# Optimization experiments

Measured on AMD Instinct MI355X. Metric: run time of the kernel, lower is better.

Reference implementation:

```python
import jax, jax.numpy as jnp
import numpy as np
from jax import lax
import math

B, C, H, W = 2, 128, 128, 256
K = 3
KK = K * K
AUX = C + 5

def conv2d(x, w, b, pad):
    out = lax.conv_general_dilated(x, w, (1, 1), [(pad, pad), (pad, pad)],
                                   dimension_numbers=('NCHW', 'OIHW', 'NCHW'))
    return out + b[None, :, None, None]

def erp_coord(h, w):
    xs = jnp.linspace(-math.pi, math.pi, w)
    ys = jnp.linspace(-math.pi / 2, math.pi / 2, h)
    theta = jnp.broadcast_to(xs[None, :], (h, w))
    phi = jnp.broadcast_to(ys[:, None], (h, w))
    return jnp.stack([jnp.sin(theta), jnp.cos(theta), jnp.sin(phi), jnp.cos(phi)], 0)[None]

def freq_energy(x, h, w):
    mag = jnp.abs(jnp.fft.rfft2(x, norm='ortho')).mean(1, keepdims=True)
    # bilinear resize (align_corners=False, half-pixel) to (h, w)
    return jax.image.resize(mag, (x.shape[0], 1, h, w), method='linear', antialias=False)

def deform_sample(x, offset):
    # x: (b,c,H,W); offset: (b, 2*KK, H, W)
    b, c, h, w = x.shape
    off = offset.reshape(b, KK, 2, h, w)
    xx = jnp.arange(w, dtype=x.dtype)[None, None, None, :]
    yy = jnp.arange(h, dtype=x.dtype)[None, None, :, None]
    # align_corners=True normalize/unnormalize cancels exactly
    px = xx + off[:, :, 0]  # (b,KK,h,w)
    py = yy + off[:, :, 1]
    x0 = jnp.floor(px).astype(jnp.int32); x1 = x0 + 1
    y0 = jnp.floor(py).astype(jnp.int32); y1 = y0 + 1
    wx1 = px - x0.astype(x.dtype); wx0 = 1.0 - wx1
    wy1 = py - y0.astype(x.dtype); wy0 = 1.0 - wy1
    flat = x.reshape(b, c, h * w)

    def gather(ix, iy):
        valid = ((ix >= 0) & (ix < w) & (iy >= 0) & (iy < h)).astype(x.dtype)
        idx = jnp.clip(iy, 0, h - 1) * w + jnp.clip(ix, 0, w - 1)  # (b,KK,h,w)
        g = jax.vmap(lambda f, i: f[:, i])(flat, idx)  # (b,c,KK,h,w)
        return g * valid[:, None]

    out = (gather(x0, y0) * (wx0 * wy0)[:, None]
           + gather(x1, y0) * (wx1 * wy0)[:, None]
           + gather(x0, y1) * (wx0 * wy1)[:, None]
           + gather(x1, y1) * (wx1 * wy1)[:, None])
    return out.reshape(b, c * KK, h, w)

def setup_inputs() -> dict:
    key = jax.random.key(0)
    ks = jax.random.split(key, 12)
    s = lambda *sh: 1.0 / np.sqrt(np.prod(sh[1:]))
    def unif(k, *sh):
        return jax.random.uniform(k, sh, jnp.float32, -s(*sh), s(*sh))
    return {
        'x': jax.random.normal(ks[0], (B, C, H, W), jnp.float32),
        'offset_w': unif(ks[1], 2 * KK, AUX, 3, 3),
        'offset_b': jnp.zeros((2 * KK,), jnp.float32),
        'gate_w1': unif(ks[2], AUX // 2, AUX, 3, 3),
        'gate_b1': jnp.zeros((AUX // 2,), jnp.float32),
        'gate_w2': unif(ks[3], 1, AUX // 2, 1, 1),
        'gate_b2': jnp.zeros((1,), jnp.float32),
        'base_w': unif(ks[4], C, C, K, K),
        'base_b': jnp.zeros((C,), jnp.float32),
        'def_w': jax.random.normal(ks[5], (C, C, K, K), jnp.float32) * s(C, C, K, K),
        'def_b': jnp.zeros((C,), jnp.float32),
    }

def reference(x, offset_w, offset_b, gate_w1, gate_b1, gate_w2, gate_b2,
              base_w, base_b, def_w, def_b):
    b, c, h, w = x.shape
    coord = jnp.broadcast_to(erp_coord(h, w), (b, 4, h, w)).astype(x.dtype)
    fe = freq_energy(x, h, w)
    aux = jnp.concatenate([x, coord, fe], 1)
    offset = conv2d(aux, offset_w, offset_b, 1)
    g = jax.nn.relu(conv2d(aux, gate_w1, gate_b1, 1))
    gate = jax.nn.sigmoid(conv2d(g, gate_w2, gate_b2, 0))
    y_base = conv2d(x, base_w, base_b, K // 2)
    sampled = deform_sample(x, offset)  # (b, c*KK, h, w)
    y_def = conv2d(sampled, def_w.reshape(c, c * KK, 1, 1), def_b, 0)
    return (1.0 - gate) * y_base + gate * y_def
```

## Files before the change

kernel.cpp:

```cpp
#include <hip/hip_runtime.h>
#include <hip/hip_bf16.h>

#define BB 2
#define CC 128
#define HH 128
#define WW 256
#define HWs (HH*WW)
#define PI_F 3.14159265358979323846f

typedef __attribute__((ext_vector_type(8))) short bf16x8;
typedef __attribute__((ext_vector_type(8))) unsigned short u16x8;
typedef __attribute__((ext_vector_type(4))) float f32x4;

__device__ __forceinline__ ushort f2bf(float f) {
  uint u = __float_as_uint(f);
  u = (u + 0x7fffu + ((u >> 16) & 1u)) >> 16;
  return (ushort)u;
}
__device__ __forceinline__ uint f2bf_fast(float f) {
  return (__float_as_uint(f) + 0x8000u) >> 16;
}
__device__ __forceinline__ float bf2f(ushort u) {
  return __uint_as_float(((uint)u) << 16);
}

__global__ __launch_bounds__(256) void pack_all_kernel(
    const float* __restrict__ bw, const float* __restrict__ dw,
    const float* __restrict__ ow, const float* __restrict__ gw,
    ushort* __restrict__ apkF, ushort* __restrict__ apkA,
    ushort* __restrict__ a1, ushort* __restrict__ a2) {
  int bid = blockIdx.x;
  int tid = threadIdx.x;
  if (bid < 144) {
    int gid = bid * 256 + tid;
    int lane = gid & 63;
    int kf = (gid >> 6) & 3;
    int mf = (gid >> 8) & 7;
    int chunk = gid >> 11;
    int part = chunk >= 9;
    int tap = part ? chunk - 9 : chunk;
    int m = mf * 16 + (lane & 15);
    int cb = kf * 32 + ((lane >> 4) << 3);
    const float* src = part ? dw : bw;
    ushort* dst = apkF + (size_t)gid * 8;
#pragma unroll
    for (int j = 0; j < 8; ++j)
      dst[j] = f2bf(src[(size_t)m * 1152 + (size_t)(cb + j) * 9 + tap]);
  } else if (bid < 212) {
    int gid = (bid - 144) * 256 + tid;
    if (gid >= 17280) return;
    int lane = gid & 63;
    int kf = (gid >> 6) % 5;
    int mf = (gid / 320) % 6;
    int tap = gid / 1920;
    int m = mf * 16 + (lane & 15);
    int cb = kf * 32 + ((lane >> 4) << 3);
#pragma unroll
    for (int j = 0; j < 8; ++j) {
      int c = cb + j;
      float v = 0.f;
      if (c < 133) {
        if (m < 18) v = ow[(size_t)m * 1197 + c * 9 + tap];
        else if (m < 84) v = gw[(size_t)(m - 18) * 1197 + c * 9 + tap];
      }
      apkA[(size_t)gid * 8 + j] = f2bf(v);
    }
  } else {
    int gid = (bid - 212) * 256 + tid;
    if (gid < 10240) {
      int lane = gid & 63, kf = (gid >> 6) & 7, mf = gid >> 9;
      int m = mf * 16 + (lane & 15);
      int kk0 = kf * 32 + ((lane >> 4) << 3);
#pragma unroll
      for (int j = 0; j < 8; ++j) {
        int kk = kk0 + j;
        float v = 0.f;
        if (m < 129)      { int tt = (m * kk) & 255;         v =  cosf(tt * (PI_F / 128.f)); }
        else if (m < 258) { int tt = ((m - 129) * kk) & 255; v = -sinf(tt * (PI_F / 128.f)); }
        a1[(size_t)gid * 8 + j] = f2bf(v);
      }
    } else if (gid < 18432) {
      int q = gid - 10240;
      int lane = q & 63, kf = (q >> 6) & 7, mf = q >> 9;
      int m = mf * 16 + (lane & 15);
      int g = m & 127;
      int kk0 = kf * 32 + ((lane >> 4) << 3);
#pragma unroll
      for (int j = 0; j < 8; ++j) {
        int kk = kk0 + j;
        int h2 = kk & 127;
        int tt = (g * h2) & 127;
        float ang = tt * (PI_F / 64.f);
        float v = (m < 128) ? ((kk < 128) ? cosf(ang) : sinf(ang))
                            : ((kk < 128) ? -sinf(ang) : cosf(ang));
        a2[(size_t)q * 8 + j] = f2bf(v);
      }
    }
  }
}

__global__ __launch_bounds__(256) void xt_kernel(const float* __restrict__ x,
    ushort* __restrict__ xt) {
  __shared__ ushort sT[64][128];
  int blk = blockIdx.x;
  int b = blk >> 7, h = blk & 127;
  int t = threadIdx.x;
  const float* xb = x + ((size_t)b * CC * HH + h) * WW;
  ushort* ob = xt + (((size_t)b * HH + h) * WW) * 128;
  for (int wt = 0; wt < 4; ++wt) {
    __syncthreads();
    {
      int w = t & 63;
      int sw = (w & 7) << 3;
#pragma unroll
      for (int it = 0; it < 4; ++it) {
        int oct = (t >> 6) + it * 4;
        u16x8 v;
#pragma unroll
        for (int j = 0; j < 8; ++j)
          v[j] = f2bf(xb[(size_t)(oct * 8 + j) * HWs + wt * 64 + w]);
        *(u16x8*)&sT[w][(oct << 3) ^ sw] = v;
      }
    }
    __syncthreads();
#pragma unroll
    for (int it = 0; it < 4; ++it) {
      int u = t + it * 256;
      int w = u >> 4, oct = u & 15;
      u16x8 v = *(const u16x8*)&sT[w][(oct << 3) ^ ((w & 7) << 3)];
      *(u16x8*)&ob[(size_t)(wt * 64 + w) * 128 + oct * 8] = v;
    }
  }
}

__global__ __launch_bounds__(256) void dft1_kernel(const float* __restrict__ x,
    const ushort* __restrict__ a1pk, ushort* __restrict__ F1) {
  int bc = blockIdx.x;
  int t = threadIdx.x, lane = t & 63, wv = t >> 6;
  int q8 = (lane >> 4) << 3, rq = (lane >> 4) << 2;
  const bf16x8* APK = (const bf16x8*)a1pk;
  ushort* f1b = F1 + (size_t)bc * 36864;
  for (int nh = 0; nh < 2; ++nh) {
    f32x4 acc[5][4];
#pragma unroll
    for (int i = 0; i < 5; ++i)
#pragma unroll
      for (int n = 0; n < 4; ++n) acc[i][n] = (f32x4){0.f, 0.f, 0.f, 0.f};
    for (int kf = 0; kf < 8; ++kf) {
      bf16x8 av[5];
#pragma unroll
      for (int i = 0; i < 5; ++i)
        av[i] = APK[(size_t)((wv * 5 + i) * 8 + kf) * 64 + lane];
#pragma unroll
      for (int n2 = 0; n2 < 4; ++n2) {
        int nf = nh * 4 + n2;
        int hh = nf * 16 + (lane & 15);
        const float* xp = x + (((size_t)bc * HH + hh) << 8) + kf * 32 + q8;
        float4 xa = *(const float4*)xp;
        float4 xb4 = *(const float4*)(xp + 4);
        bf16x8 bv;
        bv[0] = (short)f2bf(xa.x); bv[1] = (short)f2bf(xa.y);
        bv[2] = (short)f2bf(xa.z); bv[3] = (short)f2bf(xa.w);
        bv[4] = (short)f2bf(xb4.x); bv[5] = (short)f2bf(xb4.y);
        bv[6] = (short)f2bf(xb4.z); bv[7] = (short)f2bf(xb4.w);
#pragma unroll
        for (int i = 0; i < 5; ++i)
          acc[i][n2] = __builtin_amdgcn_mfma_f32_16x16x32_bf16(av[i], bv, acc[i][n2], 0, 0, 0);
      }
    }
#pragma unroll
    for (int n2 = 0; n2 < 4; ++n2) {
      int hh = (nh * 4 + n2) * 16 + (lane & 15);
#pragma unroll
      for (int i = 0; i < 5; ++i) {
#pragma unroll
        for (int r = 0; r < 4; ++r) {
          int m = (wv * 5 + i) * 16 + rq + r;
          if (m < 258) {
            int sel = m >= 129;
            int k = sel ? m - 129 : m;
            f1b[(size_t)k * 256 + sel * 128 + hh] = f2bf(acc[i][n2][r]);
          }
        }
      }
    }
  }
}

__global__ __launch_bounds__(256) void dft2_kernel(const ushort* __restrict__ F1,
    const ushort* __restrict__ a2pk, float* __restrict__ magbuf) {
  int bc = blockIdx.x;
  int t = threadIdx.x, lane = t & 63, wv = t >> 6;
  int q8 = (lane >> 4) << 3, rq = (lane >> 4) << 2;
  const bf16x8* APK = (const bf16x8*)a2pk;
  const ushort* f1b = F1 + (size_t)bc * 36864;
  float* mb = magbuf + (size_t)bc * 18432;
  for (int ng = 0; ng < 3; ++ng) {
    f32x4 acc[4][3];
#pragma unroll
    for (int i = 0; i < 4; ++i)
#pragma unroll
      for (int n = 0; n < 3; ++n) acc[i][n] = (f32x4){0.f, 0.f, 0.f, 0.f};
    for (int kf = 0; kf < 8; ++kf) {
      bf16x8 av[4];
#pragma unroll
      for (int i = 0; i < 4; ++i) {
        int mf = (i < 2) ? (2 * wv + i) : (2 * wv + (i - 2) + 8);
        av[i] = APK[(size_t)(mf * 8 + kf) * 64 + lane];
      }
#pragma unroll
      for (int n2 = 0; n2 < 3; ++n2) {
        int nf = ng * 3 + n2;
        int krow = nf * 16 + (lane & 15);
        bf16x8 bv = *(const bf16x8*)&f1b[(size_t)krow * 256 + kf * 32 + q8];
#pragma unroll
        for (int i = 0; i < 4; ++i)
          acc[i][n2] = __builtin_amdgcn_mfma_f32_16x16x32_bf16(av[i], bv, acc[i][n2], 0, 0, 0);
      }
    }
#pragma unroll
    for (int n2 = 0; n2 < 3; ++n2) {
      int k = (ng * 3 + n2) * 16 + (lane & 15);
      if (k < 129) {
#pragma unroll
        for (int pr = 0; pr < 2; ++pr) {
#pragma unroll
          for (int r = 0; r < 4; ++r) {
            int g = (2 * wv + pr) * 16 + rq + r;
            float vr = acc[pr][n2][r], vi = acc[pr + 2][n2][r];
            mb[(size_t)g * 144 + k] = sqrtf(vr * vr + vi * vi);
          }
        }
      }
    }
  }
}

__global__ __launch_bounds__(256) void fe_reduce_kernel(const float* __restrict__ magbuf,
    float* __restrict__ fe) {
  int i = blockIdx.x * 256 + threadIdx.x;
  if (i >= 36864) return;
  int k = i % 144;
  int gb = i / 144;
  int g = gb & 127, b = gb >> 7;
  if (k >= 129) return;
  const float* mp = magbuf + (size_t)b * 128 * 18432 + (size_t)g * 144 + k;
  float s = 0.f;
  for (int c = 0; c < 128; ++c) s += mp[(size_t)c * 18432];
  fe[((size_t)b * 128 + g) * 129 + k] = s * (1.0f / (181.01933598375618f * 128.0f));
}

__global__ __launch_bounds__(256) void aux_conv_kernel(
    const ushort* __restrict__ xt, const float* __restrict__ fe,
    const ushort* __restrict__ apk,
    const float* __restrict__ offset_b, const float* __restrict__ gate_b1,
    const float* __restrict__ w2, const float* __restrict__ b2,
    float* __restrict__ offs, float* __restrict__ gate) {
  __shared__ ushort Bt[64][168];
  __shared__ float gld[66][64];
  __shared__ float2 thS[66];
  __shared__ float2 phS[3];
  __shared__ float feS[3][66];
  int t = threadIdx.x;
  int bid = blockIdx.x;
  int lin = (bid & 7) * 128 + (bid >> 3);
  int bz = lin >> 9;
  int rest = lin & 511;
  int h = rest >> 2, w0 = (rest & 3) << 6;
  int lane = t & 63, wid = t >> 6;
  int wm = wid >> 1, wn = wid & 1;
  int q8 = (lane >> 4) << 3, rq = (lane >> 4) << 2;

  if (t < 66) {
    float th = -PI_F + (float)(w0 + t - 1) * (2.0f * PI_F / 255.0f);
    thS[t] = make_float2(sinf(th), cosf(th));
  }
  if (t < 3) {
    float ph = -0.5f * PI_F + (float)(h + t - 1) * (PI_F / 127.0f);
    phS[t] = make_float2(sinf(ph), cosf(ph));
  }
  if (t < 198) {
    int gyi = t / 66, gxi = t % 66;
    int gy = h + gyi - 1, gx = w0 + gxi - 1;
    float v = 0.f;
    if (gy >= 0 && gy < HH && gx >= 0 && gx < WW) {
      float sxc = ((float)gx + 0.5f) * (129.0f / 256.0f) - 0.5f;
      float fx = floorf(sxc);
      int x0 = (int)fx;
      float fr = sxc - fx;
      int x1 = min(x0 + 1, 128);
      x0 = max(x0, 0);
      const float* fb = fe + ((size_t)bz * 128 + gy) * 129;
      v = fb[x0] * (1.f - fr) + fb[x1] * fr;
    }
    feS[gyi][gxi] = v;
  }

  f32x4 acc[3][2];
#pragma unroll
  for (int i = 0; i < 3; ++i) {
    acc[i][0] = (f32x4){0.f, 0.f, 0.f, 0.f};
    acc[i][1] = (f32x4){0.f, 0.f, 0.f, 0.f};
  }
  int p0 = wn * 32 + (lane & 15), p1 = p0 + 16;
  const bf16x8* APK = (const bf16x8*)apk;
  const ushort* xtb = xt + (size_t)bz * 4194304;

  for (int tap = 0; tap < 9; ++tap) {
    int ky = tap / 3 - 1, kx = tap % 3 - 1;
    int gy = h + ky;
    __syncthreads();
    for (int u = t; u < 1280; u += 256) {
      int oct = u >> 6, p = u & 63;
      int gx = w0 + p + kx;
      bool okp = (gy >= 0) && (gy < HH) && ((unsigned)gx < 256u);
      u16x8 v = (u16x8){0, 0, 0, 0, 0, 0, 0, 0};
      if (oct < 16) {
        if (okp) v = *(const u16x8*)&xtb[((((size_t)gy << 8) + gx) << 7) + (oct << 3)];
      } else if (oct == 16) {
        if (okp) {
          float2 tc = thS[p + kx + 1];
          float2 pc = phS[ky + 1];
          float fv = feS[ky + 1][p + kx + 1];
          v[0] = f2bf(tc.x); v[1] = f2bf(tc.y);
          v[2] = f2bf(pc.x); v[3] = f2bf(pc.y);
          v[4] = f2bf(fv);
        }
      }
      *(u16x8*)&Bt[p][oct << 3] = v;
    }
    __syncthreads();
    int fb = (tap * 6 + wm * 3) * 5;
#pragma unroll
    for (int kf = 0; kf < 5; ++kf) {
      int ko = kf * 32 + q8;
      bf16x8 b0 = *(const bf16x8*)&Bt[p0][ko];
      bf16x8 b1 = *(const bf16x8*)&Bt[p1][ko];
#pragma unroll
      for (int mfi = 0; mfi < 3; ++mfi) {
        bf16x8 av = APK[(size_t)(fb + mfi * 5 + kf) * 64 + lane];
        acc[mfi][0] = __builtin_amdgcn_mfma_f32_16x16x32_bf16(av, b0, acc[mfi][0], 0, 0, 0);
        acc[mfi][1] = __builtin_amdgcn_mfma_f32_16x16x32_bf16(av, b1, acc[mfi][1], 0, 0, 0);
      }
    }
  }
#pragma unroll
  for (int nf = 0; nf < 2; ++nf) {
    int p = wn * 32 + nf * 16 + (lane & 15);
    int w = w0 + p;
#pragma unroll
    for (int mfi = 0; mfi < 3; ++mfi) {
#pragma unroll
      for (int r = 0; r < 4; ++r) {
        int oc = wm * 48 + mfi * 16 + rq + r;
        float v = acc[mfi][nf][r];
        if (oc < 18) {
          offs[((size_t)bz * 18 + oc) * HWs + h * WW + w] = v + offset_b[oc];
        } else if (oc < 84) {
          gld[oc - 18][p] = fmaxf(v + gate_b1[oc - 18], 0.f);
        }
      }
    }
  }
  __syncthreads();
  if (t < 64) {
    float s = b2[0];
    for (int c = 0; c < 66; ++c) s = fmaf(gld[c][t], w2[c], s);
    gate[(size_t)bz * HWs + h * WW + w0 + t] = 1.f / (1.f + expf(-s));
  }
}

__global__ __launch_bounds__(256) void fused_out_kernel(
    const ushort* __restrict__ xt, const float* __restrict__ offsp,
    const ushort* __restrict__ apk,
    const float* __restrict__ base_b, const float* __restrict__ def_b,
    const float* __restrict__ gate, float* __restrict__ out) {
  __shared__ ushort Win[4 * 68 * 64];
  __shared__ ushort Bt[2][64][64];
  __shared__ float gvS[64];
  __shared__ float bbS[128], bdS[128];
  int t = threadIdx.x;
  int bid = blockIdx.x;
  int lin = (bid & 7) * 128 + (bid >> 3);
  int bz = lin >> 9;
  int rest = lin & 511;
  int h = rest >> 2, w0 = (rest & 3) << 6;
  int lane = t & 63, wv = t >> 6;
  int l15 = lane & 15, lg = lane >> 4;
  int rq = lg << 2;
  const ushort* xtb = xt + (size_t)bz * 4194304;
  const bf16x8* APK = (const bf16x8*)apk;
  const u16x8 zv = (u16x8){0, 0, 0, 0, 0, 0, 0, 0};

  if (t < 64) gvS[t] = gate[(size_t)bz * HWs + h * WW + w0 + t];
  else if (t < 192) {
    int c = t - 64;
    bbS[c] = base_b[c];
    bdS[c] = def_b[c];
  }

  int p = t & 63, o4 = t >> 6;
  int mw = w0 + p;
  float oxr[9], oyr[9];
#pragma unroll
  for (int d = 0; d < 9; ++d) {
    oxr[d] = offsp[((size_t)bz * 18 + 2 * d) * HWs + h * WW + mw];
    oyr[d] = offsp[((size_t)bz * 18 + 2 * d + 1) * HWs + h * WW + mw];
  }

  f32x4 accB[2][4], accD[2][4];
#pragma unroll
  for (int mi = 0; mi < 2; ++mi)
#pragma unroll
    for (int nf = 0; nf < 4; ++nf) {
      accB[mi][nf] = (f32x4){0.f, 0.f, 0.f, 0.f};
      accD[mi][nf] = (f32x4){0.f, 0.f, 0.f, 0.f};
    }

  for (int half = 0; half < 2; ++half) {
#pragma unroll
    for (int it = 0; it < 9; ++it) {
      int u = it * 256 + t;
      if (u < 2176) {
        int s = u & 7;
        int c = (u >> 3) % 68;
        int r = u / 544;
        int gy = h - 1 + r, gx = w0 - 2 + c;
        u16x8 v = zv;
        if ((unsigned)gy < 128u && (unsigned)gx < 256u)
          v = *(const u16x8*)&xtb[((((size_t)gy << 8) + gx) << 7) + (half << 6) + (s << 3)];
        *(u16x8*)&Win[((r * 68 + c) << 6) + ((s ^ (c & 7)) << 3)] = v;
      }
    }
    __syncthreads();

    auto stage = [&](int nb, int d) {
      float px = (float)mw + oxr[d], py = (float)h + oyr[d];
      float fx = floorf(px), fy = floorf(py);
      int x0 = (int)fx, y0 = (int)fy;
      float wx1 = px - fx, wy1 = py - fy;
      float wx0 = 1.f - wx1, wy0 = 1.f - wy1;
      int x1 = x0 + 1, y1 = y0 + 1;
      bool vx0 = (unsigned)x0 < 256u, vx1 = (unsigned)x1 < 256u;
      bool vy0 = (unsigned)y0 < 128u, vy1 = (unsigned)y1 < 128u;
      float g0 = (vx0 && vy0) ? wx0 * wy0 : 0.f;
      float g1 = (vx1 && vy0) ? wx1 * wy0 : 0.f;
      float g2 = (vx0 && vy1) ? wx0 * wy1 : 0.f;
      float g3 = (vx1 && vy1) ? wx1 * wy1 : 0.f;
      int cx0 = min(max(x0, 0), 255), cx1 = min(max(x1, 0), 255);
      int cy0 = min(max(y0, 0), 127), cy1 = min(max(y1, 0), 127);
      int rx0 = cx0 - w0 + 2, rx1 = cx1 - w0 + 2;
      int ry0 = cy0 - h + 1,  ry1 = cy1 - h + 1;
      bool i00 = ((unsigned)ry0 < 4u) && ((unsigned)rx0 < 68u);
      bool i01 = ((unsigned)ry0 < 4u) && ((unsigned)rx1 < 68u);
      bool i10 = ((unsigned)ry1 < 4u) && ((unsigned)rx0 < 68u);
      bool i11 = ((unsigned)ry1 < 4u) && ((unsigned)rx1 < 68u);
#pragma unroll
      for (int oo = 0; oo < 2; ++oo) {
        int o = o4 + oo * 4;
        u16x8 v00, v01, v10, v11;
        if (i00) v00 = *(const u16x8*)&Win[((ry0 * 68 + rx0) << 6) + ((o ^ (rx0 & 7)) << 3)];
        else     v00 = *(const u16x8*)&xtb[((((size_t)cy0 << 8) + cx0) << 7) + (half << 6) + (o << 3)];
        if (i01) v01 = *(const u16x8*)&Win[((ry0 * 68 + rx1) << 6) + ((o ^ (rx1 & 7)) << 3)];
        else     v01 = *(const u16x8*)&xtb[((((size_t)cy0 << 8) + cx1) << 7) + (half << 6) + (o << 3)];
        if (i10) v10 = *(const u16x8*)&Win[((ry1 * 68 + rx0) << 6) + ((o ^ (rx0 & 7)) << 3)];
        else     v10 = *(const u16x8*)&xtb[((((size_t)cy1 << 8) + cx0) << 7) + (half << 6) + (o << 3)];
        if (i11) v11 = *(const u16x8*)&Win[((ry1 * 68 + rx1) << 6) + ((o ^ (rx1 & 7)) << 3)];
        else     v11 = *(const u16x8*)&xtb[((((size_t)cy1 << 8) + cx1) << 7) + (half << 6) + (o << 3)];
        uint pk[4];
#pragma unroll
        for (int i = 0; i < 4; ++i) {
          float f0 = bf2f(v00[2 * i]) * g0 + bf2f(v01[2 * i]) * g1
                   + bf2f(v10[2 * i]) * g2 + bf2f(v11[2 * i]) * g3;
          float f1 = bf2f(v00[2 * i + 1]) * g0 + bf2f(v01[2 * i + 1]) * g1
                   + bf2f(v10[2 * i + 1]) * g2 + bf2f(v11[2 * i + 1]) * g3;
          pk[i] = f2bf_fast(f0) | (f2bf_fast(f1) << 16);
        }
        *(uint4*)&Bt[nb][p][(o ^ (p & 7)) << 3] = make_uint4(pk[0], pk[1], pk[2], pk[3]);
      }
    };

    stage(0, 0);
    __syncthreads();

    int buf = 0;
    for (int d = 0; d < 9; ++d) {
      int ky = d / 3 - 1, kx = d % 3 - 1;
      int ryB = ky + 1;
#pragma unroll
      for (int kfi = 0; kfi < 2; ++kfi) {
        int kff = half * 2 + kfi;
        int segk = kfi * 4 + lg;
        bf16x8 aB0 = APK[(size_t)((d * 8 + wv) * 4 + kff) * 64 + lane];
        bf16x8 aB1 = APK[(size_t)((d * 8 + wv + 4) * 4 + kff) * 64 + lane];
        bf16x8 aD0 = APK[(size_t)(((9 + d) * 8 + wv) * 4 + kff) * 64 + lane];
        bf16x8 aD1 = APK[(size_t)(((9 + d) * 8 + wv + 4) * 4 + kff) * 64 + lane];
#pragma unroll
        for (int nf = 0; nf < 4; ++nf) {
          int pix = nf * 16 + l15;
          int cxr = pix + kx + 2;
          bf16x8 bB = *(const bf16x8*)&Win[((ryB * 68 + cxr) << 6) + ((segk ^ (cxr & 7)) << 3)];
          bf16x8 bD = *(const bf16x8*)&Bt[buf][pix][(segk ^ (pix & 7)) << 3];
          accB[0][nf] = __builtin_amdgcn_mfma_f32_16x16x32_bf16(aB0, bB, accB[0][nf], 0, 0, 0);
          accB[1][nf] = __builtin_amdgcn_mfma_f32_16x16x32_bf16(aB1, bB, accB[1][nf], 0, 0, 0);
          accD[0][nf] = __builtin_amdgcn_mfma_f32_16x16x32_bf16(aD0, bD, accD[0][nf], 0, 0, 0);
          accD[1][nf] = __builtin_amdgcn_mfma_f32_16x16x32_bf16(aD1, bD, accD[1][nf], 0, 0, 0);
        }
      }
      if (d < 8) stage(buf ^ 1, d + 1);
      __syncthreads();
      buf ^= 1;
    }
    if (half == 0) __syncthreads();
  }

#pragma unroll
  for (int nf = 0; nf < 4; ++nf) {
    int pix = nf * 16 + l15;
    float gv = gvS[pix], go = 1.f - gv;
    int w = w0 + pix;
#pragma unroll
    for (int mi = 0; mi < 2; ++mi) {
      int mf = wv + mi * 4;
#pragma unroll
      for (int r = 0; r < 4; ++r) {
        int oc = mf * 16 + rq + r;
        out[(((size_t)bz * CC + oc) << 15) + h * WW + w] =
            go * (accB[mi][nf][r] + bbS[oc]) + gv * (accD[mi][nf][r] + bdS[oc]);
      }
    }
  }
}

extern "C" void kernel_launch(void* const* d_in, const int* in_sizes, int n_in,
                              void* d_out, int out_size, void* d_ws, size_t ws_size,
                              hipStream_t stream) {
  const float* x        = (const float*)d_in[0];
  const float* offset_w = (const float*)d_in[1];
  const float* offset_b = (const float*)d_in[2];
  const float* gate_w1  = (const float*)d_in[3];
  const float* gate_b1  = (const float*)d_in[4];
  const float* gate_w2  = (const float*)d_in[5];
  const float* gate_b2  = (const float*)d_in[6];
  const float* base_w   = (const float*)d_in[7];
  const float* base_b   = (const float*)d_in[8];
  const float* def_w    = (const float*)d_in[9];
  const float* def_b    = (const float*)d_in[10];
  float* out = (float*)d_out;
  float* ws  = (float*)d_ws;

  float* offsb   = ws;
  float* gatebuf = offsb + 1179648;
  float* fe      = gatebuf + 65536;
  float* magbuf  = fe + 33024;
  ushort* xt     = (ushort*)(magbuf + 4718592);
  ushort* F1     = xt + 16777216;
  ushort* a1pk   = F1 + 9437184;
  ushort* a2pk   = a1pk + 81920;
  ushort* apkF   = a2pk + 65536;
  ushort* apkA   = apkF + 294912;

  pack_all_kernel<<<284, 256, 0, stream>>>(base_w, def_w, offset_w, gate_w1,
                                           apkF, apkA, a1pk, a2pk);
  xt_kernel<<<256, 256, 0, stream>>>(x, xt);

  dft1_kernel<<<256, 256, 0, stream>>>(x, a1pk, F1);
  dft2_kernel<<<256, 256, 0, stream>>>(F1, a2pk, magbuf);
  fe_reduce_kernel<<<144, 256, 0, stream>>>(magbuf, fe);

  aux_conv_kernel<<<1024, 256, 0, stream>>>(xt, fe, apkA, offset_b, gate_b1,
                                            gate_w2, gate_b2, offsb, gatebuf);

  fused_out_kernel<<<1024, 256, 0, stream>>>(xt, offsb, apkF, base_b, def_b,
                                             gatebuf, out);
}
```

Measured before the change: 196.8 us.

## Compute deformable samples directly into MFMA B-fragments, dropping shared staging buffer

The fused output kernel no longer stages bilinear-sampled values into a double-buffered shared tile with per-tap barriers. Each wave now computes the sampled B operands for its own pixels in registers and feeds them straight to MFMA. The warp tiling changes to 2x2 (64 channels by 32 pixels per wave), and offsets are cached in shared memory. This removes 9 barriers per half and the shared write/read round-trip, but each wave pair now repeats the sampling for its pixel columns, so gather and interpolation work is done twice.

```diff
diff --git a/kernel.cpp b/kernel.cpp
--- a/kernel.cpp
+++ b/kernel.cpp
@@ -376,7 +376,7 @@
     const float* __restrict__ base_b, const float* __restrict__ def_b,
     const float* __restrict__ gate, float* __restrict__ out) {
   __shared__ ushort Win[4 * 68 * 64];
-  __shared__ ushort Bt[2][64][64];
+  __shared__ float offS[9][2][64];
   __shared__ float gvS[64];
   __shared__ float bbS[128], bdS[128];
   int t = threadIdx.x;
@@ -386,6 +386,7 @@
   int rest = lin & 511;
   int h = rest >> 2, w0 = (rest & 3) << 6;
   int lane = t & 63, wv = t >> 6;
+  int wm = wv >> 1, wn = wv & 1;
   int l15 = lane & 15, lg = lane >> 4;
   int rq = lg << 2;
   const ushort* xtb = xt + (size_t)bz * 4194304;
@@ -398,26 +399,24 @@
     bbS[c] = base_b[c];
     bdS[c] = def_b[c];
   }
-
-  int p = t & 63, o4 = t >> 6;
-  int mw = w0 + p;
-  float oxr[9], oyr[9];
-#pragma unroll
-  for (int d = 0; d < 9; ++d) {
-    oxr[d] = offsp[((size_t)bz * 18 + 2 * d) * HWs + h * WW + mw];
-    oyr[d] = offsp[((size_t)bz * 18 + 2 * d + 1) * HWs + h * WW + mw];
-  }
-
-  f32x4 accB[2][4], accD[2][4];
-#pragma unroll
-  for (int mi = 0; mi < 2; ++mi)
-#pragma unroll
-    for (int nf = 0; nf < 4; ++nf) {
-      accB[mi][nf] = (f32x4){0.f, 0.f, 0.f, 0.f};
-      accD[mi][nf] = (f32x4){0.f, 0.f, 0.f, 0.f};
+  for (int u = t; u < 1152; u += 256) {
+    int d = u >> 7, r = (u >> 6) & 1, p = u & 63;
+    offS[d][r][p] = offsp[((size_t)bz * 18 + 2 * d + r) * HWs + h * WW + w0 + p];
+  }
+
+  int pix0 = wn * 32 + l15;
+
+  f32x4 acc[4][2][2];
+#pragma unroll
+  for (int i = 0; i < 4; ++i)
+#pragma unroll
+    for (int n = 0; n < 2; ++n) {
+      acc[i][n][0] = (f32x4){0.f, 0.f, 0.f, 0.f};
+      acc[i][n][1] = (f32x4){0.f, 0.f, 0.f, 0.f};
     }
 
   for (int half = 0; half < 2; ++half) {
+    if (half) __syncthreads();
 #pragma unroll
     for (int it = 0; it < 9; ++it) {
       int u = it * 256 + t;
@@ -434,99 +433,108 @@
     }
     __syncthreads();
 
-    auto stage = [&](int nb, int d) {
-      float px = (float)mw + oxr[d], py = (float)h + oyr[d];
-      float fx = floorf(px), fy = floorf(py);
-      int x0 = (int)fx, y0 = (int)fy;
-      float wx1 = px - fx, wy1 = py - fy;
-      float wx0 = 1.f - wx1, wy0 = 1.f - wy1;
-      int x1 = x0 + 1, y1 = y0 + 1;
-      bool vx0 = (unsigned)x0 < 256u, vx1 = (unsigned)x1 < 256u;
-      bool vy0 = (unsigned)y0 < 128u, vy1 = (unsigned)y1 < 128u;
-      float g0 = (vx0 && vy0) ? wx0 * wy0 : 0.f;
-      float g1 = (vx1 && vy0) ? wx1 * wy0 : 0.f;
-      float g2 = (vx0 && vy1) ? wx0 * wy1 : 0.f;
-      float g3 = (vx1 && vy1) ? wx1 * wy1 : 0.f;
-      int cx0 = min(max(x0, 0), 255), cx1 = min(max(x1, 0), 255);
-      int cy0 = min(max(y0, 0), 127), cy1 = min(max(y1, 0), 127);
-      int rx0 = cx0 - w0 + 2, rx1 = cx1 - w0 + 2;
-      int ry0 = cy0 - h + 1,  ry1 = cy1 - h + 1;
-      bool i00 = ((unsigned)ry0 < 4u) && ((unsigned)rx0 < 68u);
-      bool i01 = ((unsigned)ry0 < 4u) && ((unsigned)rx1 < 68u);
-      bool i10 = ((unsigned)ry1 < 4u) && ((unsigned)rx0 < 68u);
-      bool i11 = ((unsigned)ry1 < 4u) && ((unsigned)rx1 < 68u);
-#pragma unroll
-      for (int oo = 0; oo < 2; ++oo) {
-        int o = o4 + oo * 4;
-        u16x8 v00, v01, v10, v11;
-        if (i00) v00 = *(const u16x8*)&Win[((ry0 * 68 + rx0) << 6) + ((o ^ (rx0 & 7)) << 3)];
-        else     v00 = *(const u16x8*)&xtb[((((size_t)cy0 << 8) + cx0) << 7) + (half << 6) + (o << 3)];
-        if (i01) v01 = *(const u16x8*)&Win[((ry0 * 68 + rx1) << 6) + ((o ^ (rx1 & 7)) << 3)];
-        else     v01 = *(const u16x8*)&xtb[((((size_t)cy0 << 8) + cx1) << 7) + (half << 6) + (o << 3)];
-        if (i10) v10 = *(const u16x8*)&Win[((ry1 * 68 + rx0) << 6) + ((o ^ (rx0 & 7)) << 3)];
-        else     v10 = *(const u16x8*)&xtb[((((size_t)cy1 << 8) + cx0) << 7) + (half << 6) + (o << 3)];
-        if (i11) v11 = *(const u16x8*)&Win[((ry1 * 68 + rx1) << 6) + ((o ^ (rx1 & 7)) << 3)];
-        else     v11 = *(const u16x8*)&xtb[((((size_t)cy1 << 8) + cx1) << 7) + (half << 6) + (o << 3)];
-        uint pk[4];
-#pragma unroll
-        for (int i = 0; i < 4; ++i) {
-          float f0 = bf2f(v00[2 * i]) * g0 + bf2f(v01[2 * i]) * g1
-                   + bf2f(v10[2 * i]) * g2 + bf2f(v11[2 * i]) * g3;
-          float f1 = bf2f(v00[2 * i + 1]) * g0 + bf2f(v01[2 * i + 1]) * g1
-                   + bf2f(v10[2 * i + 1]) * g2 + bf2f(v11[2 * i + 1]) * g3;
-          pk[i] = f2bf_fast(f0) | (f2bf_fast(f1) << 16);
-        }
-        *(uint4*)&Bt[nb][p][(o ^ (p & 7)) << 3] = make_uint4(pk[0], pk[1], pk[2], pk[3]);
-      }
-    };
-
-    stage(0, 0);
-    __syncthreads();
-
-    int buf = 0;
     for (int d = 0; d < 9; ++d) {
       int ky = d / 3 - 1, kx = d % 3 - 1;
-      int ryB = ky + 1;
+      float g[2][4];
+      int wb[2][4];
+      int gb[2][4];
+      bool inw[2][4];
+#pragma unroll
+      for (int nf = 0; nf < 2; ++nf) {
+        int pix = pix0 + nf * 16;
+        float ox = offS[d][0][pix], oy = offS[d][1][pix];
+        float px = (float)(w0 + pix) + ox, py = (float)h + oy;
+        float fx = floorf(px), fy = floorf(py);
+        int x0 = (int)fx, y0 = (int)fy;
+        float wx1 = px - fx, wy1 = py - fy;
+        float wx0 = 1.f - wx1, wy0 = 1.f - wy1;
+        int x1 = x0 + 1, y1 = y0 + 1;
+        bool vx0 = (unsigned)x0 < 256u, vx1 = (unsigned)x1 < 256u;
+        bool vy0 = (unsigned)y0 < 128u, vy1 = (unsigned)y1 < 128u;
+        g[nf][0] = (vx0 && vy0) ? wx0 * wy0 : 0.f;
+        g[nf][1] = (vx1 && vy0) ? wx1 * wy0 : 0.f;
+        g[nf][2] = (vx0 && vy1) ? wx0 * wy1 : 0.f;
+        g[nf][3] = (vx1 && vy1) ? wx1 * wy1 : 0.f;
+        int cx0 = min(max(x0, 0), 255), cx1 = min(max(x1, 0), 255);
+        int cy0 = min(max(y0, 0), 127), cy1 = min(max(y1, 0), 127);
+        int rx0 = cx0 - w0 + 2, rx1 = cx1 - w0 + 2;
+        int ry0 = cy0 - h + 1,  ry1 = cy1 - h + 1;
+        inw[nf][0] = ((unsigned)ry0 < 4u) && ((unsigned)rx0 < 68u);
+        inw[nf][1] = ((unsigned)ry0 < 4u) && ((unsigned)rx1 < 68u);
+        inw[nf][2] = ((unsigned)ry1 < 4u) && ((unsigned)rx0 < 68u);
+        inw[nf][3] = ((unsigned)ry1 < 4u) && ((unsigned)rx1 < 68u);
+        wb[nf][0] = ((ry0 * 68 + rx0) << 6) ^ ((rx0 & 7) << 3);
+        wb[nf][1] = ((ry0 * 68 + rx1) << 6) ^ ((rx1 & 7) << 3);
+        wb[nf][2] = ((ry1 * 68 + rx0) << 6) ^ ((rx0 & 7) << 3);
+        wb[nf][3] = ((ry1 * 68 + rx1) << 6) ^ ((rx1 & 7) << 3);
+        gb[nf][0] = (((cy0 << 8) + cx0) << 7) + (half << 6);
+        gb[nf][1] = (((cy0 << 8) + cx1) << 7) + (half << 6);
+        gb[nf][2] = (((cy1 << 8) + cx0) << 7) + (half << 6);
+        gb[nf][3] = (((cy1 << 8) + cx1) << 7) + (half << 6);
+      }
 #pragma unroll
       for (int kfi = 0; kfi < 2; ++kfi) {
+        int o = kfi * 4 + lg;
+        int o8 = o << 3;
+        bf16x8 bD[2], bB[2];
+#pragma unroll
+        for (int nf = 0; nf < 2; ++nf) {
+          u16x8 cv[4];
+#pragma unroll
+          for (int c = 0; c < 4; ++c) {
+            if (inw[nf][c]) cv[c] = *(const u16x8*)&Win[wb[nf][c] ^ o8];
+            else            cv[c] = *(const u16x8*)&xtb[gb[nf][c] + o8];
+          }
+          uint pk[4];
+#pragma unroll
+          for (int i = 0; i < 4; ++i) {
+            float f0 = bf2f(cv[0][2 * i]) * g[nf][0] + bf2f(cv[1][2 * i]) * g[nf][1]
+                     + bf2f(cv[2][2 * i]) * g[nf][2] + bf2f(cv[3][2 * i]) * g[nf][3];
+            float f1 = bf2f(cv[0][2 * i + 1]) * g[nf][0] + bf2f(cv[1][2 * i + 1]) * g[nf][1]
+                     + bf2f(cv[2][2 * i + 1]) * g[nf][2] + bf2f(cv[3][2 * i + 1]) * g[nf][3];
+            pk[i] = f2bf_fast(f0) | (f2bf_fast(f1) << 16);
+          }
+          uint4 tmp = make_uint4(pk[0], pk[1], pk[2], pk[3]);
+          bD[nf] = *(const bf16x8*)&tmp;
+          int cxr = pix0 + nf * 16 + kx + 2;
+          bB[nf] = *(const bf16x8*)&Win[(((ky + 1) * 68 + cxr) << 6) + ((o ^ (cxr & 7)) << 3)];
+        }
         int kff = half * 2 + kfi;
-        int segk = kfi * 4 + lg;
-        bf16x8 aB0 = APK[(size_t)((d * 8 + wv) * 4 + kff) * 64 + lane];
-        bf16x8 aB1 = APK[(size_t)((d * 8 + wv + 4) * 4 + kff) * 64 + lane];
-        bf16x8 aD0 = APK[(size_t)(((9 + d) * 8 + wv) * 4 + kff) * 64 + lane];
-        bf16x8 aD1 = APK[(size_t)(((9 + d) * 8 + wv + 4) * 4 + kff) * 64 + lane];
-#pragma unroll
-        for (int nf = 0; nf < 4; ++nf) {
-          int pix = nf * 16 + l15;
-          int cxr = pix + kx + 2;
-          bf16x8 bB = *(const bf16x8*)&Win[((ryB * 68 + cxr) << 6) + ((segk ^ (cxr & 7)) << 3)];
-          bf16x8 bD = *(const bf16x8*)&Bt[buf][pix][(segk ^ (pix & 7)) << 3];
-          accB[0][nf] = __builtin_amdgcn_mfma_f32_16x16x32_bf16(aB0, bB, accB[0][nf], 0, 0, 0);
-          accB[1][nf] = __builtin_amdgcn_mfma_f32_16x16x32_bf16(aB1, bB, accB[1][nf], 0, 0, 0);
-          accD[0][nf] = __builtin_amdgcn_mfma_f32_16x16x32_bf16(aD0, bD, accD[0][nf], 0, 0, 0);
-          accD[1][nf] = __builtin_amdgcn_mfma_f32_16x16x32_bf16(aD1, bD, accD[1][nf], 0, 0, 0);
-        }
-      }
-      if (d < 8) stage(buf ^ 1, d + 1);
-      __syncthreads();
-      buf ^= 1;
-    }
-    if (half == 0) __syncthreads();
-  }
-
-#pragma unroll
-  for (int nf = 0; nf < 4; ++nf) {
-    int pix = nf * 16 + l15;
+        {
+          int cb = d * 8;
+#pragma unroll
+          for (int mfi = 0; mfi < 4; ++mfi) {
+            bf16x8 av = APK[(size_t)((cb + wm * 4 + mfi) * 4 + kff) * 64 + lane];
+            acc[mfi][0][0] = __builtin_amdgcn_mfma_f32_16x16x32_bf16(av, bB[0], acc[mfi][0][0], 0, 0, 0);
+            acc[mfi][1][0] = __builtin_amdgcn_mfma_f32_16x16x32_bf16(av, bB[1], acc[mfi][1][0], 0, 0, 0);
+          }
+        }
+        {
+          int cb = (9 + d) * 8;
+#pragma unroll
+          for (int mfi = 0; mfi < 4; ++mfi) {
+            bf16x8 av = APK[(size_t)((cb + wm * 4 + mfi) * 4 + kff) * 64 + lane];
+            acc[mfi][0][1] = __builtin_amdgcn_mfma_f32_16x16x32_bf16(av, bD[0], acc[mfi][0][1], 0, 0, 0);
+            acc[mfi][1][1] = __builtin_amdgcn_mfma_f32_16x16x32_bf16(av, bD[1], acc[mfi][1][1], 0, 0, 0);
+          }
+        }
+      }
+    }
+  }
+
+#pragma unroll
+  for (int nf = 0; nf < 2; ++nf) {
+    int pix = pix0 + nf * 16;
     float gv = gvS[pix], go = 1.f - gv;
     int w = w0 + pix;
 #pragma unroll
-    for (int mi = 0; mi < 2; ++mi) {
-      int mf = wv + mi * 4;
+    for (int mfi = 0; mfi < 4; ++mfi) {
+      int mfr = wm * 4 + mfi;
 #pragma unroll
       for (int r = 0; r < 4; ++r) {
-        int oc = mf * 16 + rq + r;
+        int oc = mfr * 16 + rq + r;
         out[(((size_t)bz * CC + oc) << 15) + h * WW + w] =
-            go * (accB[mi][nf][r] + bbS[oc]) + gv * (accD[mi][nf][r] + bdS[oc]);
+            go * (acc[mfi][nf][0][r] + bbS[oc]) + gv * (acc[mfi][nf][1][r] + bdS[oc]);
       }
     }
   }
```

Result: slower. 221.8 us (+12.7%).

## Split deform sampling into prefetch/combine stages overlapping MFMA, pack bilinear math, raise occupancy

Applied to the files above, without the earlier changes.

Splits the deformable sampling stage into a load phase, issued before the MFMA loop for the current tap, and a combine/write phase issued after it, so gather latency from LDS and global memory overlaps the matrix work. The bilinear combine now uses packed float2 arithmetic with simplified bf16 unpacking and packing. It also adds a 3-blocks-per-CU launch bound and fully unrolls the half and tap loops. Keeping the prefetched data live across the MFMA loop raises register pressure, which the occupancy hint may turn into spills.

```diff
diff --git a/kernel.cpp b/kernel.cpp
--- a/kernel.cpp
+++ b/kernel.cpp
@@ -11,17 +11,26 @@
 typedef __attribute__((ext_vector_type(8))) short bf16x8;
 typedef __attribute__((ext_vector_type(8))) unsigned short u16x8;
 typedef __attribute__((ext_vector_type(4))) float f32x4;
+typedef __attribute__((ext_vector_type(2))) float f32x2;
 
 __device__ __forceinline__ ushort f2bf(float f) {
   uint u = __float_as_uint(f);
   u = (u + 0x7fffu + ((u >> 16) & 1u)) >> 16;
   return (ushort)u;
 }
-__device__ __forceinline__ uint f2bf_fast(float f) {
-  return (__float_as_uint(f) + 0x8000u) >> 16;
-}
 __device__ __forceinline__ float bf2f(ushort u) {
   return __uint_as_float(((uint)u) << 16);
+}
+__device__ __forceinline__ uint comb4(uint u0, uint u1, uint u2, uint u3,
+                                      f32x2 g0, f32x2 g1, f32x2 g2, f32x2 g3) {
+  f32x2 a0 = (f32x2){__uint_as_float(u0 << 16), __uint_as_float(u0 & 0xffff0000u)};
+  f32x2 a1 = (f32x2){__uint_as_float(u1 << 16), __uint_as_float(u1 & 0xffff0000u)};
+  f32x2 a2 = (f32x2){__uint_as_float(u2 << 16), __uint_as_float(u2 & 0xffff0000u)};
+  f32x2 a3 = (f32x2){__uint_as_float(u3 << 16), __uint_as_float(u3 & 0xffff0000u)};
+  f32x2 s = a0 * g0 + a1 * g1 + a2 * g2 + a3 * g3;
+  uint ua = __float_as_uint(s.x) + 0x8000u;
+  uint ub = __float_as_uint(s.y) + 0x8000u;
+  return (ua >> 16) | (ub & 0xffff0000u);
 }
 
 __global__ __launch_bounds__(256) void pack_all_kernel(
@@ -370,7 +379,7 @@
   }
 }
 
-__global__ __launch_bounds__(256) void fused_out_kernel(
+__global__ __launch_bounds__(256, 3) void fused_out_kernel(
     const ushort* __restrict__ xt, const float* __restrict__ offsp,
     const ushort* __restrict__ apk,
     const float* __restrict__ base_b, const float* __restrict__ def_b,
@@ -390,7 +399,6 @@
   int rq = lg << 2;
   const ushort* xtb = xt + (size_t)bz * 4194304;
   const bf16x8* APK = (const bf16x8*)apk;
-  const u16x8 zv = (u16x8){0, 0, 0, 0, 0, 0, 0, 0};
 
   if (t < 64) gvS[t] = gate[(size_t)bz * HWs + h * WW + w0 + t];
   else if (t < 192) {
@@ -417,7 +425,9 @@
       accD[mi][nf] = (f32x4){0.f, 0.f, 0.f, 0.f};
     }
 
+#pragma unroll
   for (int half = 0; half < 2; ++half) {
+    if (half) __syncthreads();
 #pragma unroll
     for (int it = 0; it < 9; ++it) {
       int u = it * 256 + t;
@@ -426,7 +436,7 @@
         int c = (u >> 3) % 68;
         int r = u / 544;
         int gy = h - 1 + r, gx = w0 - 2 + c;
-        u16x8 v = zv;
+        u16x8 v = (u16x8){0, 0, 0, 0, 0, 0, 0, 0};
         if ((unsigned)gy < 128u && (unsigned)gx < 256u)
           v = *(const u16x8*)&xtb[((((size_t)gy << 8) + gx) << 7) + (half << 6) + (s << 3)];
         *(u16x8*)&Win[((r * 68 + c) << 6) + ((s ^ (c & 7)) << 3)] = v;
@@ -434,7 +444,9 @@
     }
     __syncthreads();
 
-    auto stage = [&](int nb, int d) {
+    uint4 q[2][4];
+    f32x2 gw4[4];
+    auto stage_load = [&](int d) {
       float px = (float)mw + oxr[d], py = (float)h + oyr[d];
       float fx = floorf(px), fy = floorf(py);
       int x0 = (int)fx, y0 = (int)fy;
@@ -447,44 +459,61 @@
       float g1 = (vx1 && vy0) ? wx1 * wy0 : 0.f;
       float g2 = (vx0 && vy1) ? wx0 * wy1 : 0.f;
       float g3 = (vx1 && vy1) ? wx1 * wy1 : 0.f;
+      gw4[0] = (f32x2){g0, g0}; gw4[1] = (f32x2){g1, g1};
+      gw4[2] = (f32x2){g2, g2}; gw4[3] = (f32x2){g3, g3};
       int cx0 = min(max(x0, 0), 255), cx1 = min(max(x1, 0), 255);
       int cy0 = min(max(y0, 0), 127), cy1 = min(max(y1, 0), 127);
       int rx0 = cx0 - w0 + 2, rx1 = cx1 - w0 + 2;
       int ry0 = cy0 - h + 1,  ry1 = cy1 - h + 1;
-      bool i00 = ((unsigned)ry0 < 4u) && ((unsigned)rx0 < 68u);
-      bool i01 = ((unsigned)ry0 < 4u) && ((unsigned)rx1 < 68u);
-      bool i10 = ((unsigned)ry1 < 4u) && ((unsigned)rx0 < 68u);
-      bool i11 = ((unsigned)ry1 < 4u) && ((unsigned)rx1 < 68u);
+      bool inw[4];
+      inw[0] = ((unsigned)ry0 < 4u) && ((unsigned)rx0 < 68u);
+      inw[1] = ((unsigned)ry0 < 4u) && ((unsigned)rx1 < 68u);
+      inw[2] = ((unsigned)ry1 < 4u) && ((unsigned)rx0 < 68u);
+      inw[3] = ((unsigned)ry1 < 4u) && ((unsigned)rx1 < 68u);
+      int wb[4];
+      wb[0] = ((ry0 * 68 + rx0) << 6) ^ ((rx0 & 7) << 3);
+      wb[1] = ((ry0 * 68 + rx1) << 6) ^ ((rx1 & 7) << 3);
+      wb[2] = ((ry1 * 68 + rx0) << 6) ^ ((rx0 & 7) << 3);
+      wb[3] = ((ry1 * 68 + rx1) << 6) ^ ((rx1 & 7) << 3);
+      int gb[4];
+      gb[0] = (((cy0 << 8) + cx0) << 7) + (half << 6);
+      gb[1] = (((cy0 << 8) + cx1) << 7) + (half << 6);
+      gb[2] = (((cy1 << 8) + cx0) << 7) + (half << 6);
+      gb[3] = (((cy1 << 8) + cx1) << 7) + (half << 6);
 #pragma unroll
       for (int oo = 0; oo < 2; ++oo) {
+        int o8 = (o4 + oo * 4) << 3;
+#pragma unroll
+        for (int c = 0; c < 4; ++c) {
+          if (inw[c]) q[oo][c] = *(const uint4*)&Win[wb[c] ^ o8];
+          else        q[oo][c] = *(const uint4*)&xtb[gb[c] + o8];
+        }
+      }
+    };
+    auto stage_write = [&](int nb) {
+#pragma unroll
+      for (int oo = 0; oo < 2; ++oo) {
+        uint4 r;
+        r.x = comb4(q[oo][0].x, q[oo][1].x, q[oo][2].x, q[oo][3].x,
+                    gw4[0], gw4[1], gw4[2], gw4[3]);
+        r.y = comb4(q[oo][0].y, q[oo][1].y, q[oo][2].y, q[oo][3].y,
+                    gw4[0], gw4[1], gw4[2], gw4[3]);
+        r.z = comb4(q[oo][0].z, q[oo][1].z, q[oo][2].z, q[oo][3].z,
+                    gw4[0], gw4[1], gw4[2], gw4[3]);
+        r.w = comb4(q[oo][0].w, q[oo][1].w, q[oo][2].w, q[oo][3].w,
+                    gw4[0], gw4[1], gw4[2], gw4[3]);
         int o = o4 + oo * 4;
-        u16x8 v00, v01, v10, v11;
-        if (i00) v00 = *(const u16x8*)&Win[((ry0 * 68 + rx0) << 6) + ((o ^ (rx0 & 7)) << 3)];
-        else     v00 = *(const u16x8*)&xtb[((((size_t)cy0 << 8) + cx0) << 7) + (half << 6) + (o << 3)];
-        if (i01) v01 = *(const u16x8*)&Win[((ry0 * 68 + rx1) << 6) + ((o ^ (rx1 & 7)) << 3)];
-        else     v01 = *(const u16x8*)&xtb[((((size_t)cy0 << 8) + cx1) << 7) + (half << 6) + (o << 3)];
-        if (i10) v10 = *(const u16x8*)&Win[((ry1 * 68 + rx0) << 6) + ((o ^ (rx0 & 7)) << 3)];
-        else     v10 = *(const u16x8*)&xtb[((((size_t)cy1 << 8) + cx0) << 7) + (half << 6) + (o << 3)];
-        if (i11) v11 = *(const u16x8*)&Win[((ry1 * 68 + rx1) << 6) + ((o ^ (rx1 & 7)) << 3)];
-        else     v11 = *(const u16x8*)&xtb[((((size_t)cy1 << 8) + cx1) << 7) + (half << 6) + (o << 3)];
-        uint pk[4];
-#pragma unroll
-        for (int i = 0; i < 4; ++i) {
-          float f0 = bf2f(v00[2 * i]) * g0 + bf2f(v01[2 * i]) * g1
-                   + bf2f(v10[2 * i]) * g2 + bf2f(v11[2 * i]) * g3;
-          float f1 = bf2f(v00[2 * i + 1]) * g0 + bf2f(v01[2 * i + 1]) * g1
-                   + bf2f(v10[2 * i + 1]) * g2 + bf2f(v11[2 * i + 1]) * g3;
-          pk[i] = f2bf_fast(f0) | (f2bf_fast(f1) << 16);
-        }
-        *(uint4*)&Bt[nb][p][(o ^ (p & 7)) << 3] = make_uint4(pk[0], pk[1], pk[2], pk[3]);
+        *(uint4*)&Bt[nb][p][(o ^ (p & 7)) << 3] = r;
       }
     };
 
-    stage(0, 0);
+    stage_load(0);
+    stage_write(0);
     __syncthreads();
 
-    int buf = 0;
+#pragma unroll
     for (int d = 0; d < 9; ++d) {
+      if (d < 8) stage_load(d + 1);
       int ky = d / 3 - 1, kx = d % 3 - 1;
       int ryB = ky + 1;
 #pragma unroll
@@ -500,18 +529,16 @@
           int pix = nf * 16 + l15;
           int cxr = pix + kx + 2;
           bf16x8 bB = *(const bf16x8*)&Win[((ryB * 68 + cxr) << 6) + ((segk ^ (cxr & 7)) << 3)];
-          bf16x8 bD = *(const bf16x8*)&Bt[buf][pix][(segk ^ (pix & 7)) << 3];
+          bf16x8 bD = *(const bf16x8*)&Bt[d & 1][pix][(segk ^ (pix & 7)) << 3];
           accB[0][nf] = __builtin_amdgcn_mfma_f32_16x16x32_bf16(aB0, bB, accB[0][nf], 0, 0, 0);
           accB[1][nf] = __builtin_amdgcn_mfma_f32_16x16x32_bf16(aB1, bB, accB[1][nf], 0, 0, 0);
           accD[0][nf] = __builtin_amdgcn_mfma_f32_16x16x32_bf16(aD0, bD, accD[0][nf], 0, 0, 0);
           accD[1][nf] = __builtin_amdgcn_mfma_f32_16x16x32_bf16(aD1, bD, accD[1][nf], 0, 0, 0);
         }
       }
-      if (d < 8) stage(buf ^ 1, d + 1);
+      if (d < 8) stage_write((d + 1) & 1);
       __syncthreads();
-      buf ^= 1;
-    }
-    if (half == 0) __syncthreads();
+    }
   }
 
 #pragma unroll
```

Measured after the change: 532.9 us. 171% more time.
